# Performance work log

Hardware: AMD Instinct MI355X
Metric: run time of the kernel (lower is better)

## Reference

```python
import jax, jax.numpy as jnp
import numpy as np

IN_CH = 256
OUT_CH = 256
RED = 4
QK = OUT_CH // RED  # 64


def setup_inputs() -> dict:
    key = jax.random.key(0)
    ks = jax.random.split(key, 7)
    s = 1.0 / np.sqrt(IN_CH)
    return {
        "x": jax.random.normal(ks[0], (8, IN_CH, 64, 64), dtype=jnp.float32),
        "w_q": jax.random.uniform(ks[1], (QK, IN_CH), jnp.float32, -s, s),
        "b_q": jax.random.uniform(ks[2], (QK,), jnp.float32, -s, s),
        "w_k": jax.random.uniform(ks[3], (QK, IN_CH), jnp.float32, -s, s),
        "b_k": jax.random.uniform(ks[4], (QK,), jnp.float32, -s, s),
        "w_v": jax.random.uniform(ks[5], (OUT_CH, IN_CH), jnp.float32, -s, s),
        "b_v": jax.random.uniform(ks[6], (OUT_CH,), jnp.float32, -s, s),
    }


def reference(x, w_q, b_q, w_k, b_k, w_v, b_v):
    B, C, H, W = x.shape
    xt = x.reshape(B, C, H * W)  # [B, C, N]
    # 1x1 convs == channel matmuls
    q = jnp.einsum('dc,bcn->bnd', w_q, xt) + b_q  # [B, N, QK]
    k = jnp.einsum('dc,bcn->bdn', w_k, xt) + b_k[:, None]  # [B, QK, N]
    v = jnp.einsum('dc,bcn->bnd', w_v, xt) + b_v  # [B, N, OUT]
    scores = jnp.einsum('bnd,bdm->bnm', q, k)  # [B, N, N], no scaling (as in source)
    attn = jax.nn.softmax(scores, axis=-1)
    out = jnp.einsum('bnm,bmd->bdn', attn, v)  # [B, OUT, N]
    return out.reshape(B, -1, H, W)
```

## Files before the change

kernel.cpp:

```cpp
#include <hip/hip_runtime.h>

typedef __bf16 bf16x8 __attribute__((ext_vector_type(8)));
typedef float f32x4 __attribute__((ext_vector_type(4)));
typedef unsigned int u32;
typedef unsigned short u16;

#define LOG2E 1.44269504088896f

__device__ __forceinline__ u16 f2bf(float f){
  u32 b = __builtin_bit_cast(u32, f);
  b += 0x7FFFu + ((b >> 16) & 1u);
  return (u16)(b >> 16);
}

__global__ void prep_w(const float* __restrict__ wq, const float* __restrict__ wk,
                       const float* __restrict__ wv, u16* __restrict__ wfrag){
  int idx  = blockIdx.x * 256 + threadIdx.x;
  int e    = idx & 7;
  int lane = (idx >> 3) & 63;
  int f    = idx >> 9;
  int cc = f / 24, dt = f % 24;
  int d = dt * 16 + (lane & 15);
  int c = cc * 32 + (lane >> 4) * 8 + e;
  float v;
  if (d < 64)       v = wq[d * 256 + c];
  else if (d < 128) v = wk[(d - 64) * 256 + c];
  else              v = wv[(d - 128) * 256 + c];
  wfrag[idx] = f2bf(v);
}

__launch_bounds__(256, 2)
__global__ void proj_kernel(const float* __restrict__ x,
                            const float* __restrict__ bq, const float* __restrict__ bk,
                            const float* __restrict__ bv,
                            const u16* __restrict__ wfrag,
                            u16* __restrict__ qb, u16* __restrict__ kb, u16* __restrict__ vt)
{
  __shared__ u16 xlds[64 * 256];
  const int b    = blockIdx.x & 7;
  const int n0   = (blockIdx.x >> 3) * 64;
  const int t    = threadIdx.x;
  const int lane = t & 63;
  const int w    = t >> 6;
  const int g    = lane >> 4, j = lane & 15;

  {
    const int n = t & 63;
    const float* xp = x + ((size_t)b * 256) * 4096 + n0 + n;
    char* lbase = reinterpret_cast<char*>(xlds);
    #pragma unroll
    for (int pass = 0; pass < 8; ++pass){
      int c = pass * 32 + (t >> 6) * 8;
      float f0 = xp[(size_t)(c+0)*4096], f1 = xp[(size_t)(c+1)*4096];
      float f2 = xp[(size_t)(c+2)*4096], f3 = xp[(size_t)(c+3)*4096];
      float f4 = xp[(size_t)(c+4)*4096], f5 = xp[(size_t)(c+5)*4096];
      float f6 = xp[(size_t)(c+6)*4096], f7 = xp[(size_t)(c+7)*4096];
      uint4 q;
      q.x = (u32)f2bf(f0) | ((u32)f2bf(f1) << 16);
      q.y = (u32)f2bf(f2) | ((u32)f2bf(f3) << 16);
      q.z = (u32)f2bf(f4) | ((u32)f2bf(f5) << 16);
      q.w = (u32)f2bf(f6) | ((u32)f2bf(f7) << 16);
      u32 off = (u32)n * 512 + (((u32)c * 2) ^ (((u32)n & 31) << 4));
      *reinterpret_cast<uint4*>(lbase + off) = q;
    }
  }
  __syncthreads();

  f32x4 acc[6][4];
  #pragma unroll
  for (int i = 0; i < 6; ++i)
    #pragma unroll
    for (int nt = 0; nt < 4; ++nt) acc[i][nt] = f32x4{0.f,0.f,0.f,0.f};

  const char* lbase = reinterpret_cast<const char*>(xlds);
  for (int cc = 0; cc < 8; ++cc){
    bf16x8 a[6];
    #pragma unroll
    for (int i = 0; i < 6; ++i)
      a[i] = *reinterpret_cast<const bf16x8*>(wfrag + ((size_t)(cc*24 + w*6 + i) * 64 + lane) * 8);
    bf16x8 bb[4];
    #pragma unroll
    for (int nt = 0; nt < 4; ++nt){
      const u32 row = nt * 16 + j;
      const u32 off = row * 512 + (((u32)(cc * 64 + g * 16)) ^ ((row & 31) << 4));
      bb[nt] = *reinterpret_cast<const bf16x8*>(lbase + off);
    }
    #pragma unroll
    for (int i = 0; i < 6; ++i)
      #pragma unroll
      for (int nt = 0; nt < 4; ++nt)
        acc[i][nt] = __builtin_amdgcn_mfma_f32_16x16x32_bf16(a[i], bb[nt], acc[i][nt], 0, 0, 0);
  }

  #pragma unroll
  for (int i = 0; i < 6; ++i){
    const int dt = w * 6 + i;
    const int d0 = dt * 16;
    const int dd = d0 + 4 * g;
    if (d0 < 64){
      float b0 = bq[dd], b1 = bq[dd+1], b2 = bq[dd+2], b3 = bq[dd+3];
      #pragma unroll
      for (int nt = 0; nt < 4; ++nt){
        const int n = n0 + nt * 16 + j;
        uint2 u;
        u.x = (u32)f2bf(acc[i][nt][0] + b0) | ((u32)f2bf(acc[i][nt][1] + b1) << 16);
        u.y = (u32)f2bf(acc[i][nt][2] + b2) | ((u32)f2bf(acc[i][nt][3] + b3) << 16);
        *reinterpret_cast<uint2*>(qb + ((size_t)b * 4096 + n) * 64 + dd) = u;
      }
    } else if (d0 < 128){
      const int dk = dd - 64;
      float b0 = bk[dk], b1 = bk[dk+1], b2 = bk[dk+2], b3 = bk[dk+3];
      #pragma unroll
      for (int nt = 0; nt < 4; ++nt){
        const int n = n0 + nt * 16 + j;
        uint2 u;
        u.x = (u32)f2bf(acc[i][nt][0] + b0) | ((u32)f2bf(acc[i][nt][1] + b1) << 16);
        u.y = (u32)f2bf(acc[i][nt][2] + b2) | ((u32)f2bf(acc[i][nt][3] + b3) << 16);
        *reinterpret_cast<uint2*>(kb + ((size_t)b * 4096 + n) * 64 + dk) = u;
      }
    } else {
      const int dv = dd - 128;
      float b0 = bv[dv], b1 = bv[dv+1], b2 = bv[dv+2], b3 = bv[dv+3];
      #pragma unroll
      for (int nt = 0; nt < 4; ++nt){
        const int n = n0 + nt * 16 + j;
        u16* vp = vt + (size_t)b * 256 * 4096 + n;
        vp[(size_t)(dv+0) * 4096] = f2bf(acc[i][nt][0] + b0);
        vp[(size_t)(dv+1) * 4096] = f2bf(acc[i][nt][1] + b1);
        vp[(size_t)(dv+2) * 4096] = f2bf(acc[i][nt][2] + b2);
        vp[(size_t)(dv+3) * 4096] = f2bf(acc[i][nt][3] + b3);
      }
    }
  }
}

__launch_bounds__(512, 2)
__global__ void attn_kernel(const u16* __restrict__ qb, const u16* __restrict__ kb,
                            const u16* __restrict__ vt, float* __restrict__ out)
{
  __shared__ u16 kl[2][64 * 64];
  __shared__ u16 vl[2][256 * 64];
  __shared__ u16 pl[8][16 * 64];

  const int b    = blockIdx.x & 7;
  const int qc   = blockIdx.x >> 3;
  const int t    = threadIdx.x, lane = t & 63, w = t >> 6;
  const int g    = lane >> 4, j = lane & 15;

  const u16* Kg = kb + (size_t)b * 4096 * 64;
  const u16* Vg = vt + (size_t)b * 256 * 4096;

  const u16* Qrow = qb + ((size_t)b * 4096 + qc * 128 + w * 16 + j) * 64;
  const bf16x8 qf0 = *reinterpret_cast<const bf16x8*>(Qrow + 8 * g);
  const bf16x8 qf1 = *reinterpret_cast<const bf16x8*>(Qrow + 32 + 8 * g);

  f32x4 o[16];
  #pragma unroll
  for (int i = 0; i < 16; ++i) o[i] = f32x4{0.f,0.f,0.f,0.f};
  float mrun = -3.0e38f, lrun = 0.f;

  auto stage = [&](int tile, int buf){
    const int m0 = tile * 64;
    {
      const int r = w * 8 + (lane >> 3);
      const char* src = reinterpret_cast<const char*>(Kg + (size_t)(m0 + r) * 64)
                        + ((((u32)lane & 7) * 16) ^ ((((u32)r) & 7) << 4));
      char* dst = reinterpret_cast<char*>(&kl[buf][0]) + w * 1024;
      __builtin_amdgcn_global_load_lds((const __attribute__((address_space(1))) void*)src,
                                       (__attribute__((address_space(3))) void*)dst, 16, 0, 0);
    }
    #pragma unroll
    for (int i = 0; i < 4; ++i){
      const int dv = w * 32 + i * 8 + (lane >> 3);
      const char* src = reinterpret_cast<const char*>(Vg + (size_t)dv * 4096 + m0)
                        + ((((u32)lane & 7) * 16) ^ (((u32)dv & 7) << 4));
      char* dst = reinterpret_cast<char*>(&vl[buf][0]) + (w * 32 + i * 8) * 128;
      __builtin_amdgcn_global_load_lds((const __attribute__((address_space(1))) void*)src,
                                       (__attribute__((address_space(3))) void*)dst, 16, 0, 0);
    }
  };

  stage(0, 0);
  __syncthreads();

  char* pbase = reinterpret_cast<char*>(&pl[w][0]);

  for (int tile = 0; tile < 64; ++tile){
    const int cur = tile & 1;
    if (tile + 1 < 64) stage(tile + 1, cur ^ 1);

    const char* kbase = reinterpret_cast<const char*>(&kl[cur][0]);
    const char* vbase = reinterpret_cast<const char*>(&vl[cur][0]);

    f32x4 s[4];
    #pragma unroll
    for (int mt = 0; mt < 4; ++mt){
      const u32 row = mt * 16 + j;
      const u32 sw  = (row & 7) << 4;
      bf16x8 ka0 = *reinterpret_cast<const bf16x8*>(kbase + row * 128 + (((u32)(g * 16)) ^ sw));
      bf16x8 ka1 = *reinterpret_cast<const bf16x8*>(kbase + row * 128 + (((u32)(64 + g * 16)) ^ sw));
      f32x4 z = f32x4{0.f,0.f,0.f,0.f};
      z = __builtin_amdgcn_mfma_f32_16x16x32_bf16(ka0, qf0, z, 0, 0, 0);
      z = __builtin_amdgcn_mfma_f32_16x16x32_bf16(ka1, qf1, z, 0, 0, 0);
      s[mt] = z;
    }

    float pmax = s[0][0];
    #pragma unroll
    for (int mt = 0; mt < 4; ++mt)
      #pragma unroll
      for (int r = 0; r < 4; ++r) pmax = fmaxf(pmax, s[mt][r]);
    pmax = fmaxf(pmax, __shfl_xor(pmax, 16));
    pmax = fmaxf(pmax, __shfl_xor(pmax, 32));

    const float mnew  = fmaxf(mrun, pmax);
    const float alpha = exp2f((mrun - mnew) * LOG2E);
    mrun = mnew;

    float psum = 0.f;
    u32 pk[8];
    #pragma unroll
    for (int mt = 0; mt < 4; ++mt){
      float p0 = exp2f((s[mt][0] - mnew) * LOG2E);
      float p1 = exp2f((s[mt][1] - mnew) * LOG2E);
      float p2 = exp2f((s[mt][2] - mnew) * LOG2E);
      float p3 = exp2f((s[mt][3] - mnew) * LOG2E);
      psum += (p0 + p1) + (p2 + p3);
      pk[2*mt]   = (u32)f2bf(p0) | ((u32)f2bf(p1) << 16);
      pk[2*mt+1] = (u32)f2bf(p2) | ((u32)f2bf(p3) << 16);
    }
    psum += __shfl_xor(psum, 16);
    psum += __shfl_xor(psum, 32);
    lrun = lrun * alpha + psum;

    #pragma unroll
    for (int i = 0; i < 16; ++i){
      o[i][0] *= alpha; o[i][1] *= alpha; o[i][2] *= alpha; o[i][3] *= alpha;
    }

    {
      const u32 swp = ((u32)j & 7) << 4;
      #pragma unroll
      for (int mt = 0; mt < 4; ++mt){
        uint2 u; u.x = pk[2*mt]; u.y = pk[2*mt+1];
        *reinterpret_cast<uint2*>(pbase + (u32)j * 128 + (((u32)(mt * 32 + 8 * g)) ^ swp)) = u;
      }
    }

    #pragma unroll
    for (int mc = 0; mc < 2; ++mc){
      const u32 swp = ((u32)j & 7) << 4;
      bf16x8 pf = *reinterpret_cast<const bf16x8*>(pbase + (u32)j * 128 + (((u32)(mc * 64 + 16 * g)) ^ swp));
      #pragma unroll
      for (int dt = 0; dt < 16; ++dt){
        const u32 dv = dt * 16 + j;
        bf16x8 vf = *reinterpret_cast<const bf16x8*>(vbase + dv * 128 + (((u32)(mc * 64 + 16 * g)) ^ ((dv & 7) << 4)));
        o[dt] = __builtin_amdgcn_mfma_f32_16x16x32_bf16(vf, pf, o[dt], 0, 0, 0);
      }
    }

    __syncthreads();
  }

  const float rinv = 1.0f / lrun;
  const int n = qc * 128 + w * 16 + j;
  float* ob = out + (size_t)b * 256 * 4096 + n;
  #pragma unroll
  for (int dt = 0; dt < 16; ++dt){
    const int dv0 = dt * 16 + 4 * g;
    #pragma unroll
    for (int r = 0; r < 4; ++r)
      ob[(size_t)(dv0 + r) * 4096] = o[dt][r] * rinv;
  }
}

extern "C" void kernel_launch(void* const* d_in, const int* in_sizes, int n_in,
                              void* d_out, int out_size, void* d_ws, size_t ws_size,
                              hipStream_t stream)
{
  (void)in_sizes; (void)n_in; (void)out_size; (void)ws_size;
  const float* x  = (const float*)d_in[0];
  const float* wq = (const float*)d_in[1];
  const float* bq = (const float*)d_in[2];
  const float* wk = (const float*)d_in[3];
  const float* bk = (const float*)d_in[4];
  const float* wv = (const float*)d_in[5];
  const float* bv = (const float*)d_in[6];
  float* out = (float*)d_out;

  char* ws = (char*)d_ws;
  u16* qbuf  = (u16*)(ws + 0);
  u16* kbuf  = (u16*)(ws + 4194304);
  u16* vbuf  = (u16*)(ws + 8388608);
  u16* wfrag = (u16*)(ws + 25165824);

  prep_w<<<dim3(384), dim3(256), 0, stream>>>(wq, wk, wv, wfrag);
  proj_kernel<<<dim3(512), dim3(256), 0, stream>>>(x, bq, bk, bv, wfrag, qbuf, kbuf, vbuf);
  attn_kernel<<<dim3(256), dim3(512), 0, stream>>>(qbuf, kbuf, vbuf, out);
}
```

Before: 263.6 us.

## Keep P in registers via V column permutation, lazy rescale, smaller blocks

The projection kernel folds log2(e) into Q and stores V with its columns permuted within each 64-wide tile, so the P fragment from the score MFMA can feed the PV MFMA straight from registers. That removes the per-wave LDS round trip for P. The online softmax now skips rescaling unless the row max grows by more than 8 (in log2 units) and uses the raw hardware exp2. The attention launch changes from 256 blocks of 512 threads to 512 blocks of 256 threads, and s_setprio hints are added around the MFMA sections. The lazy rescale lets unnormalized exponentials grow to about 2^8 before correction, which slightly loosens the numerical bounds.

```diff
diff --git a/kernel.cpp b/kernel.cpp
--- a/kernel.cpp
+++ b/kernel.cpp
@@ -3,6 +3,7 @@
 typedef __bf16 bf16x8 __attribute__((ext_vector_type(8)));
 typedef float f32x4 __attribute__((ext_vector_type(4)));
 typedef unsigned int u32;
+typedef u32 u32x4v __attribute__((ext_vector_type(4)));
 typedef unsigned short u16;
 
 #define LOG2E 1.44269504088896f
@@ -103,8 +104,8 @@
       for (int nt = 0; nt < 4; ++nt){
         const int n = n0 + nt * 16 + j;
         uint2 u;
-        u.x = (u32)f2bf(acc[i][nt][0] + b0) | ((u32)f2bf(acc[i][nt][1] + b1) << 16);
-        u.y = (u32)f2bf(acc[i][nt][2] + b2) | ((u32)f2bf(acc[i][nt][3] + b3) << 16);
+        u.x = (u32)f2bf((acc[i][nt][0] + b0) * LOG2E) | ((u32)f2bf((acc[i][nt][1] + b1) * LOG2E) << 16);
+        u.y = (u32)f2bf((acc[i][nt][2] + b2) * LOG2E) | ((u32)f2bf((acc[i][nt][3] + b3) * LOG2E) << 16);
         *reinterpret_cast<uint2*>(qb + ((size_t)b * 4096 + n) * 64 + dd) = u;
       }
     } else if (d0 < 128){
@@ -123,7 +124,8 @@
       float b0 = bv[dv], b1 = bv[dv+1], b2 = bv[dv+2], b3 = bv[dv+3];
       #pragma unroll
       for (int nt = 0; nt < 4; ++nt){
-        const int n = n0 + nt * 16 + j;
+        const int scol = ((nt & 2) << 4) | ((j & 12) << 1) | ((nt & 1) << 2) | (j & 3);
+        const int n = n0 + scol;
         u16* vp = vt + (size_t)b * 256 * 4096 + n;
         vp[(size_t)(dv+0) * 4096] = f2bf(acc[i][nt][0] + b0);
         vp[(size_t)(dv+1) * 4096] = f2bf(acc[i][nt][1] + b1);
@@ -134,13 +136,12 @@
   }
 }
 
-__launch_bounds__(512, 2)
+__launch_bounds__(256, 2)
 __global__ void attn_kernel(const u16* __restrict__ qb, const u16* __restrict__ kb,
                             const u16* __restrict__ vt, float* __restrict__ out)
 {
   __shared__ u16 kl[2][64 * 64];
   __shared__ u16 vl[2][256 * 64];
-  __shared__ u16 pl[8][16 * 64];
 
   const int b    = blockIdx.x & 7;
   const int qc   = blockIdx.x >> 3;
@@ -150,31 +151,32 @@
   const u16* Kg = kb + (size_t)b * 4096 * 64;
   const u16* Vg = vt + (size_t)b * 256 * 4096;
 
-  const u16* Qrow = qb + ((size_t)b * 4096 + qc * 128 + w * 16 + j) * 64;
+  const u16* Qrow = qb + ((size_t)b * 4096 + qc * 64 + w * 16 + j) * 64;
   const bf16x8 qf0 = *reinterpret_cast<const bf16x8*>(Qrow + 8 * g);
   const bf16x8 qf1 = *reinterpret_cast<const bf16x8*>(Qrow + 32 + 8 * g);
 
   f32x4 o[16];
   #pragma unroll
   for (int i = 0; i < 16; ++i) o[i] = f32x4{0.f,0.f,0.f,0.f};
-  float mrun = -3.0e38f, lrun = 0.f;
+  float mrun = -1.0e30f, lrun = 0.f;
 
   auto stage = [&](int tile, int buf){
     const int m0 = tile * 64;
-    {
-      const int r = w * 8 + (lane >> 3);
+    #pragma unroll
+    for (int i = 0; i < 2; ++i){
+      const int r = i * 32 + w * 8 + (lane >> 3);
       const char* src = reinterpret_cast<const char*>(Kg + (size_t)(m0 + r) * 64)
                         + ((((u32)lane & 7) * 16) ^ ((((u32)r) & 7) << 4));
-      char* dst = reinterpret_cast<char*>(&kl[buf][0]) + w * 1024;
+      char* dst = reinterpret_cast<char*>(&kl[buf][0]) + i * 4096 + w * 1024;
       __builtin_amdgcn_global_load_lds((const __attribute__((address_space(1))) void*)src,
                                        (__attribute__((address_space(3))) void*)dst, 16, 0, 0);
     }
     #pragma unroll
-    for (int i = 0; i < 4; ++i){
-      const int dv = w * 32 + i * 8 + (lane >> 3);
+    for (int i = 0; i < 8; ++i){
+      const int dv = i * 32 + w * 8 + (lane >> 3);
       const char* src = reinterpret_cast<const char*>(Vg + (size_t)dv * 4096 + m0)
                         + ((((u32)lane & 7) * 16) ^ (((u32)dv & 7) << 4));
-      char* dst = reinterpret_cast<char*>(&vl[buf][0]) + (w * 32 + i * 8) * 128;
+      char* dst = reinterpret_cast<char*>(&vl[buf][0]) + i * 4096 + w * 1024;
       __builtin_amdgcn_global_load_lds((const __attribute__((address_space(1))) void*)src,
                                        (__attribute__((address_space(3))) void*)dst, 16, 0, 0);
     }
@@ -183,7 +185,7 @@
   stage(0, 0);
   __syncthreads();
 
-  char* pbase = reinterpret_cast<char*>(&pl[w][0]);
+  const u32 vsw = ((u32)j & 7) << 4;
 
   for (int tile = 0; tile < 64; ++tile){
     const int cur = tile & 1;
@@ -193,6 +195,7 @@
     const char* vbase = reinterpret_cast<const char*>(&vl[cur][0]);
 
     f32x4 s[4];
+    __builtin_amdgcn_s_setprio(1);
     #pragma unroll
     for (int mt = 0; mt < 4; ++mt){
       const u32 row = mt * 16 + j;
@@ -204,6 +207,7 @@
       z = __builtin_amdgcn_mfma_f32_16x16x32_bf16(ka1, qf1, z, 0, 0, 0);
       s[mt] = z;
     }
+    __builtin_amdgcn_s_setprio(0);
 
     float pmax = s[0][0];
     #pragma unroll
@@ -213,57 +217,52 @@
     pmax = fmaxf(pmax, __shfl_xor(pmax, 16));
     pmax = fmaxf(pmax, __shfl_xor(pmax, 32));
 
-    const float mnew  = fmaxf(mrun, pmax);
-    const float alpha = exp2f((mrun - mnew) * LOG2E);
-    mrun = mnew;
+    if (__any(pmax > mrun + 8.0f)){
+      const float mnew  = fmaxf(mrun, pmax);
+      const float alpha = __builtin_amdgcn_exp2f(mrun - mnew);
+      mrun = mnew;
+      lrun *= alpha;
+      #pragma unroll
+      for (int i = 0; i < 16; ++i){
+        o[i][0] *= alpha; o[i][1] *= alpha; o[i][2] *= alpha; o[i][3] *= alpha;
+      }
+    }
 
     float psum = 0.f;
     u32 pk[8];
     #pragma unroll
     for (int mt = 0; mt < 4; ++mt){
-      float p0 = exp2f((s[mt][0] - mnew) * LOG2E);
-      float p1 = exp2f((s[mt][1] - mnew) * LOG2E);
-      float p2 = exp2f((s[mt][2] - mnew) * LOG2E);
-      float p3 = exp2f((s[mt][3] - mnew) * LOG2E);
+      float p0 = __builtin_amdgcn_exp2f(s[mt][0] - mrun);
+      float p1 = __builtin_amdgcn_exp2f(s[mt][1] - mrun);
+      float p2 = __builtin_amdgcn_exp2f(s[mt][2] - mrun);
+      float p3 = __builtin_amdgcn_exp2f(s[mt][3] - mrun);
       psum += (p0 + p1) + (p2 + p3);
       pk[2*mt]   = (u32)f2bf(p0) | ((u32)f2bf(p1) << 16);
       pk[2*mt+1] = (u32)f2bf(p2) | ((u32)f2bf(p3) << 16);
     }
     psum += __shfl_xor(psum, 16);
     psum += __shfl_xor(psum, 32);
-    lrun = lrun * alpha + psum;
-
-    #pragma unroll
-    for (int i = 0; i < 16; ++i){
-      o[i][0] *= alpha; o[i][1] *= alpha; o[i][2] *= alpha; o[i][3] *= alpha;
-    }
-
-    {
-      const u32 swp = ((u32)j & 7) << 4;
-      #pragma unroll
-      for (int mt = 0; mt < 4; ++mt){
-        uint2 u; u.x = pk[2*mt]; u.y = pk[2*mt+1];
-        *reinterpret_cast<uint2*>(pbase + (u32)j * 128 + (((u32)(mt * 32 + 8 * g)) ^ swp)) = u;
-      }
-    }
-
+    lrun += psum;
+
+    __builtin_amdgcn_s_setprio(1);
     #pragma unroll
     for (int mc = 0; mc < 2; ++mc){
-      const u32 swp = ((u32)j & 7) << 4;
-      bf16x8 pf = *reinterpret_cast<const bf16x8*>(pbase + (u32)j * 128 + (((u32)(mc * 64 + 16 * g)) ^ swp));
+      u32x4v pw = { pk[4*mc+0], pk[4*mc+1], pk[4*mc+2], pk[4*mc+3] };
+      bf16x8 pf = __builtin_bit_cast(bf16x8, pw);
       #pragma unroll
       for (int dt = 0; dt < 16; ++dt){
         const u32 dv = dt * 16 + j;
-        bf16x8 vf = *reinterpret_cast<const bf16x8*>(vbase + dv * 128 + (((u32)(mc * 64 + 16 * g)) ^ ((dv & 7) << 4)));
+        bf16x8 vf = *reinterpret_cast<const bf16x8*>(vbase + dv * 128 + (((u32)(mc * 64 + 16 * g)) ^ vsw));
         o[dt] = __builtin_amdgcn_mfma_f32_16x16x32_bf16(vf, pf, o[dt], 0, 0, 0);
       }
     }
+    __builtin_amdgcn_s_setprio(0);
 
     __syncthreads();
   }
 
   const float rinv = 1.0f / lrun;
-  const int n = qc * 128 + w * 16 + j;
+  const int n = qc * 64 + w * 16 + j;
   float* ob = out + (size_t)b * 256 * 4096 + n;
   #pragma unroll
   for (int dt = 0; dt < 16; ++dt){
@@ -296,5 +295,5 @@
 
   prep_w<<<dim3(384), dim3(256), 0, stream>>>(wq, wk, wv, wfrag);
   proj_kernel<<<dim3(512), dim3(256), 0, stream>>>(x, bq, bk, bv, wfrag, qbuf, kbuf, vbuf);
-  attn_kernel<<<dim3(256), dim3(512), 0, stream>>>(qbuf, kbuf, vbuf, out);
-}
+  attn_kernel<<<dim3(512), dim3(256), 0, stream>>>(qbuf, kbuf, vbuf, out);
+}
```

New measurement: 221.6 us. 16.0% less time.
